# Kernel tuning notes

Measured on AMD Instinct MI355X. Metric: run time of the kernel, lower is better.

## Reference

```python
import jax, jax.numpy as jnp
import numpy as np

B, N, D, H = 64, 512, 1024, 2048


def setup_inputs() -> dict:
    key = jax.random.key(0)
    k1, k2, k3, k4, k5 = jax.random.split(key, 5)
    s1 = 1.0 / np.sqrt(D)
    s2 = 1.0 / np.sqrt(H)
    return {
        "x": jax.random.normal(k1, (B, N, D), dtype=jnp.float32),
        "W1": jax.random.uniform(k2, (H, D), jnp.float32, -s1, s1),
        "b1": jax.random.uniform(k3, (H,), jnp.float32, -s1, s1),
        "W2": jax.random.uniform(k4, (1, H), jnp.float32, -s2, s2),
        "b2": jax.random.uniform(k5, (1,), jnp.float32, -s2, s2),
    }


def reference(x, W1, b1, W2, b2):
    # energy gate: sigmoid(sum(x^2)) over feature dim -> [B, N]
    energy_weights = jax.nn.sigmoid(jnp.sum(x * x, axis=-1))
    # fused per-node MLP as one batched GEMM: relu(x @ W1^T + b1) @ W2^T + b2
    hidden = jax.nn.relu(jnp.einsum("bnd,hd->bnh", x, W1) + b1)
    score = jnp.einsum("bnh,oh->bno", hidden, W2)[..., 0] + b2[0]  # [B, N]
    attn_weights = jax.nn.sigmoid(score) * energy_weights  # [B, N]
    # diag_embed: place attn_weights on the diagonal of [B, N, N]
    filter_matrix = attn_weights[:, :, None] * jnp.eye(N, dtype=x.dtype)
    return filter_matrix, attn_weights
```

## Files before the change

### kernel.cpp

```cpp
#include <hip/hip_runtime.h>
#include <hip/hip_bf16.h>

#define Bc 64
#define Nc 512
#define Dc 1024
#define Hc 2048
#define Mc (Bc * Nc)

#define BM 256
#define BH 256
#define BK 64
#define KTILES (Dc / BK)
#define MTILES (Mc / BM)
#define HTILES (Hc / BH)
#define NSLICE (HTILES * 4)

typedef __attribute__((ext_vector_type(8))) short bf16x8;
typedef __attribute__((ext_vector_type(4))) float f32x4;

__device__ __forceinline__ unsigned short f2bf(float f) {
    unsigned u = __float_as_uint(f);
    u += 0x7FFFu + ((u >> 16) & 1u);
    return (unsigned short)(u >> 16);
}

__device__ __forceinline__ void stage16(const void* g, void* l) {
    __builtin_amdgcn_global_load_lds(
        (const __attribute__((address_space(1))) unsigned int*)g,
        (__attribute__((address_space(3))) unsigned int*)l,
        16, 0, 0);
}

__global__ void __launch_bounds__(256) cast_fused(
    const float* __restrict__ x, const float* __restrict__ w1,
    unsigned short* __restrict__ xb, unsigned short* __restrict__ w1b,
    float* __restrict__ energy)
{
    const int tid = threadIdx.x;
    if (blockIdx.x < Mc / 8) {
        const int row0 = blockIdx.x * 8 + (tid >> 6) * 2;
        const int lane = tid & 63;
        const float4* s0 = (const float4*)(x + (size_t)row0 * Dc);
        const float4* s1 = (const float4*)(x + (size_t)(row0 + 1) * Dc);
        ushort4* d0 = (ushort4*)(xb + (size_t)row0 * Dc);
        ushort4* d1 = (ushort4*)(xb + (size_t)(row0 + 1) * Dc);
        float4 v0[4], v1[4];
        #pragma unroll
        for (int j = 0; j < 4; ++j) v0[j] = s0[lane + j * 64];
        #pragma unroll
        for (int j = 0; j < 4; ++j) v1[j] = s1[lane + j * 64];
        float a = 0.0f, bsum = 0.0f;
        #pragma unroll
        for (int j = 0; j < 4; ++j) {
            ushort4 o;
            o.x = f2bf(v0[j].x); o.y = f2bf(v0[j].y);
            o.z = f2bf(v0[j].z); o.w = f2bf(v0[j].w);
            d0[lane + j * 64] = o;
            a += v0[j].x * v0[j].x + v0[j].y * v0[j].y +
                 v0[j].z * v0[j].z + v0[j].w * v0[j].w;
        }
        #pragma unroll
        for (int j = 0; j < 4; ++j) {
            ushort4 o;
            o.x = f2bf(v1[j].x); o.y = f2bf(v1[j].y);
            o.z = f2bf(v1[j].z); o.w = f2bf(v1[j].w);
            d1[lane + j * 64] = o;
            bsum += v1[j].x * v1[j].x + v1[j].y * v1[j].y +
                    v1[j].z * v1[j].z + v1[j].w * v1[j].w;
        }
        #pragma unroll
        for (int m = 1; m < 64; m <<= 1) {
            a    += __shfl_xor(a, m);
            bsum += __shfl_xor(bsum, m);
        }
        if (lane == 0) {
            energy[row0]     = 1.0f / (1.0f + expf(-a));
            energy[row0 + 1] = 1.0f / (1.0f + expf(-bsum));
        }
    } else {
        const size_t i = (size_t)(blockIdx.x - Mc / 8) * 256 + tid;
        const float4 v = ((const float4*)w1)[i];
        ushort4 o;
        o.x = f2bf(v.x); o.y = f2bf(v.y); o.z = f2bf(v.z); o.w = f2bf(v.w);
        ((ushort4*)w1b)[i] = o;
    }
}

__global__ void __launch_bounds__(512, 2) fused_gemm_score(
    const unsigned short* __restrict__ xb,
    const unsigned short* __restrict__ w1b,
    const float* __restrict__ b1,
    const float* __restrict__ w2,
    float* __restrict__ score_part,
    float* __restrict__ zf)
{
    extern __shared__ __attribute__((aligned(16))) unsigned short lds[];

    const int tid  = threadIdx.x;
    const int lane = tid & 63;
    const int wid  = tid >> 6;
    const int wr   = wid >> 2;
    const int wc   = wid & 3;
    const int l15  = lane & 15;
    const int l4   = lane >> 4;

    const int b  = blockIdx.x;
    const int wg = (b & 7) * (MTILES * HTILES / 8) + (b >> 3);
    const int mt = wg >> 3;
    const int ht = wg & 7;
    const int m0 = mt * BM;
    const int h0 = ht * BH;

    float b1v[4], w2v[4];
    #pragma unroll
    for (int n = 0; n < 4; ++n) {
        const int h = h0 + wc * 64 + n * 16 + l15;
        b1v[n] = b1[h];
        w2v[n] = w2[h];
    }

    const int srow    = tid >> 3;
    const int scol_sw = ((((tid & 7) * 16) ^ ((srow & 7) << 4)) >> 1);

    unsigned short* A0p = lds;
    #define LDSBUF(buf, mat) (A0p + (buf) * 32768 + (mat) * 16384)

    const int swz   = (l15 & 7) << 4;
    const int offk0 = ((l4 * 16) ^ swz);
    const int offk1 = ((64 + l4 * 16) ^ swz);
    const int arow  = (wr * 128 + l15) * 128;
    const int brow  = (wc * 64 + l15) * 128;

#define RD_A(dst, bf, mh) { \
    _Pragma("unroll") for (int mf = 0; mf < 4; ++mf) { \
        dst[mf][0] = *(const bf16x8*)((char*)LDSBUF(bf, 0) + arow + ((mh)*64 + mf*16) * 128 + offk0); \
        dst[mf][1] = *(const bf16x8*)((char*)LDSBUF(bf, 0) + arow + ((mh)*64 + mf*16) * 128 + offk1); } }
#define RD_B(dst, bf, nh) { \
    _Pragma("unroll") for (int nf = 0; nf < 2; ++nf) { \
        dst[nf][0] = *(const bf16x8*)((char*)LDSBUF(bf, 1) + brow + ((nh)*32 + nf*16) * 128 + offk0); \
        dst[nf][1] = *(const bf16x8*)((char*)LDSBUF(bf, 1) + brow + ((nh)*32 + nf*16) * 128 + offk1); } }

#define MMQ(av, bv, mh, nh) { \
    _Pragma("unroll") for (int mf = 0; mf < 4; ++mf) \
    _Pragma("unroll") for (int nf = 0; nf < 2; ++nf) { \
        acc[(mh)*4+mf][(nh)*2+nf] = __builtin_amdgcn_mfma_f32_16x16x32_bf16( \
            av[mf][0], bv[nf][0], acc[(mh)*4+mf][(nh)*2+nf], 0, 0, 0); \
        acc[(mh)*4+mf][(nh)*2+nf] = __builtin_amdgcn_mfma_f32_16x16x32_bf16( \
            av[mf][1], bv[nf][1], acc[(mh)*4+mf][(nh)*2+nf], 0, 0, 0); } }

    f32x4 acc[8][4];
    #pragma unroll
    for (int m = 0; m < 8; ++m)
        #pragma unroll
        for (int n = 0; n < 4; ++n) acc[m][n] = (f32x4)(0.0f);

    f32x4* zbase = zf ? (f32x4*)(zf + (size_t)b * 16384 + tid * 4) : nullptr;
    const f32x4 zero4 = (f32x4)(0.0f);

    #pragma unroll
    for (int c = 0; c < 4; ++c) {
        stage16(xb  + (size_t)(m0 + c * 64 + srow) * Dc + scol_sw,
                ((char*)LDSBUF(0, 0)) + c * 8192 + tid * 16);
        stage16(w1b + (size_t)(h0 + c * 64 + srow) * Dc + scol_sw,
                ((char*)LDSBUF(0, 1)) + c * 8192 + tid * 16);
    }
    __syncthreads();

    int cur = 0;
    for (int kt = 0; kt < KTILES; ++kt) {
        if (kt + 1 < KTILES) {
            const int k0 = (kt + 1) * BK;
            const int nb = cur ^ 1;
            #pragma unroll
            for (int c = 0; c < 4; ++c) {
                stage16(xb  + (size_t)(m0 + c * 64 + srow) * Dc + k0 + scol_sw,
                        ((char*)LDSBUF(nb, 0)) + c * 8192 + tid * 16);
                stage16(w1b + (size_t)(h0 + c * 64 + srow) * Dc + k0 + scol_sw,
                        ((char*)LDSBUF(nb, 1)) + c * 8192 + tid * 16);
            }
        }

        if (zbase && kt >= 8)
            __builtin_nontemporal_store(zero4, zbase + (size_t)(kt - 8) * 512);

        bf16x8 a0[4][2], a1[4][2], b0[2][2], b1f[2][2];

        RD_A(a0, cur, 0); RD_B(b0, cur, 0);
        RD_B(b1f, cur, 1);
        MMQ(a0, b0, 0, 0);
        RD_A(a1, cur, 1);
        MMQ(a0, b1f, 0, 1);
        MMQ(a1, b1f, 1, 1);
        MMQ(a1, b0, 1, 0);

        __syncthreads();
        cur ^= 1;
    }

    float sp[8][4];
    #pragma unroll
    for (int m = 0; m < 8; ++m)
        #pragma unroll
        for (int j = 0; j < 4; ++j) sp[m][j] = 0.0f;
    #pragma unroll
    for (int n = 0; n < 4; ++n)
        #pragma unroll
        for (int m = 0; m < 8; ++m)
            #pragma unroll
            for (int j = 0; j < 4; ++j) {
                float v = acc[m][n][j] + b1v[n];
                v = v > 0.0f ? v : 0.0f;
                sp[m][j] += v * w2v[n];
            }

    #pragma unroll
    for (int m = 0; m < 8; ++m)
        #pragma unroll
        for (int j = 0; j < 4; ++j) {
            float v = sp[m][j];
            v += __shfl_xor(v, 1);
            v += __shfl_xor(v, 2);
            v += __shfl_xor(v, 4);
            v += __shfl_xor(v, 8);
            sp[m][j] = v;
        }

    if (l15 == 0) {
        const size_t base = (size_t)(ht * 4 + wc) * Mc;
        #pragma unroll
        for (int m = 0; m < 8; ++m)
            #pragma unroll
            for (int j = 0; j < 4; ++j) {
                const int row = m0 + wr * 128 + m * 16 + l4 * 4 + j;
                score_part[base + row] = sp[m][j];
            }
    }
}

__global__ void __launch_bounds__(256) finalize_scatter(
    const float* __restrict__ score_part, const float* __restrict__ energy,
    const float* __restrict__ b2, float* __restrict__ out)
{
    const int row = blockIdx.x * 256 + threadIdx.x;
    float s = b2[0];
    #pragma unroll
    for (int g = 0; g < NSLICE; ++g) s += score_part[(size_t)g * Mc + row];
    const float attn = (1.0f / (1.0f + expf(-s))) * energy[row];
    const int bb = row >> 9;
    const int n  = row & (Nc - 1);
    out[(size_t)bb * Nc * Nc + (size_t)n * (Nc + 1)] = attn;
    out[(size_t)Bc * Nc * Nc + row] = attn;
}

__global__ void __launch_bounds__(256) finalize_full(
    const float* __restrict__ score_part, const float* __restrict__ energy,
    const float* __restrict__ b2, float* __restrict__ out)
{
    const int row = blockIdx.x * 2 + (threadIdx.x >> 7);
    const int t   = threadIdx.x & 127;

    float s = b2[0];
    #pragma unroll
    for (int g = 0; g < NSLICE; ++g) s += score_part[(size_t)g * Mc + row];
    const float attn = (1.0f / (1.0f + expf(-s))) * energy[row];

    const int n = row & (Nc - 1);
    float4 z = make_float4(0.0f, 0.0f, 0.0f, 0.0f);
    if (t == (n >> 2)) ((float*)&z)[n & 3] = attn;
    ((float4*)(out + (size_t)row * Nc))[t] = z;
    if (t == 0) out[(size_t)Bc * Nc * Nc + row] = attn;
}

extern "C" void kernel_launch(void* const* d_in, const int* in_sizes, int n_in,
                              void* d_out, int out_size, void* d_ws, size_t ws_size,
                              hipStream_t stream) {
    const float* x  = (const float*)d_in[0];
    const float* W1 = (const float*)d_in[1];
    const float* b1 = (const float*)d_in[2];
    const float* W2 = (const float*)d_in[3];
    const float* b2 = (const float*)d_in[4];
    float* out = (float*)d_out;

    const size_t xb_bytes = (size_t)Mc * Dc * 2;
    const size_t w1_bytes = (size_t)Hc * Dc * 2;
    const size_t e_bytes  = (size_t)Mc * 4;
    const size_t s_bytes  = (size_t)NSLICE * Mc * 4;

    char* ws = (char*)d_ws;
    unsigned short* xb;
    bool xb_in_out = false;
    if (ws_size >= xb_bytes + w1_bytes + e_bytes + s_bytes + 256) {
        xb = (unsigned short*)ws; ws += xb_bytes;
    } else {
        xb = (unsigned short*)d_out;
        xb_in_out = true;
    }
    unsigned short* w1b = (unsigned short*)ws; ws += w1_bytes;
    float* energy = (float*)ws; ws += e_bytes;
    float* score  = (float*)ws; ws += s_bytes;

    const int w1_blocks = (Hc * Dc / 4) / 256;
    cast_fused<<<Mc / 8 + w1_blocks, 256, 0, stream>>>(x, W1, xb, w1b, energy);
    fused_gemm_score<<<MTILES * HTILES, 512, 131072, stream>>>(
        xb, w1b, b1, W2, score, xb_in_out ? nullptr : out);
    if (xb_in_out)
        finalize_full<<<Mc / 2, 256, 0, stream>>>(score, energy, b2, out);
    else
        finalize_scatter<<<Mc / 256, 256, 0, stream>>>(score, energy, b2, out);
}
```

Baseline: 151.7 us.

## Use 4 waves with 128x128 per-wave tiles in fused GEMM-score kernel

Restructures the 256x256 block GEMM from 8 waves of 128x64 to 4 waves of 128x128 each, raising per-wave register reuse of B fragments (read once per k-step, reused across 8 A row groups). Staging is redistributed over 256 threads, the zero-store of the output is spread across all 16 k-tiles, and the number of score partial slices halves. This doubles accumulator registers per thread (256 floats) and drops to one workgroup per CU with fewer waves to hide latency, risking spills or lower occupancy.

New measurement: 169.8 us. 11.9% more time.

```diff
diff --git a/kernel.cpp b/kernel.cpp
--- a/kernel.cpp
+++ b/kernel.cpp
@@ -13,7 +13,7 @@
 #define KTILES (Dc / BK)
 #define MTILES (Mc / BM)
 #define HTILES (Hc / BH)
-#define NSLICE (HTILES * 4)
+#define NSLICE (HTILES * 2)
 
 typedef __attribute__((ext_vector_type(8))) short bf16x8;
 typedef __attribute__((ext_vector_type(4))) float f32x4;
@@ -86,7 +86,7 @@
     }
 }
 
-__global__ void __launch_bounds__(512, 2) fused_gemm_score(
+__global__ void __launch_bounds__(256, 1) fused_gemm_score(
     const unsigned short* __restrict__ xb,
     const unsigned short* __restrict__ w1b,
     const float* __restrict__ b1,
@@ -94,13 +94,13 @@
     float* __restrict__ score_part,
     float* __restrict__ zf)
 {
-    extern __shared__ __attribute__((aligned(16))) unsigned short lds[];
+    extern __shared__ __attribute__((aligned(16))) char lds[];
 
     const int tid  = threadIdx.x;
     const int lane = tid & 63;
     const int wid  = tid >> 6;
-    const int wr   = wid >> 2;
-    const int wc   = wid & 3;
+    const int wr   = wid >> 1;
+    const int wc   = wid & 1;
     const int l15  = lane & 15;
     const int l4   = lane >> 4;
 
@@ -111,10 +111,10 @@
     const int m0 = mt * BM;
     const int h0 = ht * BH;
 
-    float b1v[4], w2v[4];
-    #pragma unroll
-    for (int n = 0; n < 4; ++n) {
-        const int h = h0 + wc * 64 + n * 16 + l15;
+    float b1v[8], w2v[8];
+    #pragma unroll
+    for (int n = 0; n < 8; ++n) {
+        const int h = h0 + wc * 128 + n * 16 + l15;
         b1v[n] = b1[h];
         w2v[n] = w2[h];
     }
@@ -122,76 +122,71 @@
     const int srow    = tid >> 3;
     const int scol_sw = ((((tid & 7) * 16) ^ ((srow & 7) << 4)) >> 1);
 
-    unsigned short* A0p = lds;
-    #define LDSBUF(buf, mat) (A0p + (buf) * 32768 + (mat) * 16384)
+#define LDSA(bf) (lds + (bf) * 65536)
+#define LDSB(bf) (lds + (bf) * 65536 + 32768)
+
+#define STG_A(bf, kt) { \
+    const unsigned short* _g = xb + (size_t)(m0 + srow) * Dc + (kt) * BK + scol_sw; \
+    _Pragma("unroll") for (int c = 0; c < 8; ++c) \
+        stage16(_g + (size_t)c * 32 * Dc, LDSA(bf) + c * 4096 + tid * 16); }
+#define STG_B(bf, kt) { \
+    const unsigned short* _g = w1b + (size_t)(h0 + srow) * Dc + (kt) * BK + scol_sw; \
+    _Pragma("unroll") for (int c = 0; c < 8; ++c) \
+        stage16(_g + (size_t)c * 32 * Dc, LDSB(bf) + c * 4096 + tid * 16); }
 
     const int swz   = (l15 & 7) << 4;
     const int offk0 = ((l4 * 16) ^ swz);
     const int offk1 = ((64 + l4 * 16) ^ swz);
-    const int arow  = (wr * 128 + l15) * 128;
-    const int brow  = (wc * 64 + l15) * 128;
-
-#define RD_A(dst, bf, mh) { \
-    _Pragma("unroll") for (int mf = 0; mf < 4; ++mf) { \
-        dst[mf][0] = *(const bf16x8*)((char*)LDSBUF(bf, 0) + arow + ((mh)*64 + mf*16) * 128 + offk0); \
-        dst[mf][1] = *(const bf16x8*)((char*)LDSBUF(bf, 0) + arow + ((mh)*64 + mf*16) * 128 + offk1); } }
-#define RD_B(dst, bf, nh) { \
-    _Pragma("unroll") for (int nf = 0; nf < 2; ++nf) { \
-        dst[nf][0] = *(const bf16x8*)((char*)LDSBUF(bf, 1) + brow + ((nh)*32 + nf*16) * 128 + offk0); \
-        dst[nf][1] = *(const bf16x8*)((char*)LDSBUF(bf, 1) + brow + ((nh)*32 + nf*16) * 128 + offk1); } }
-
-#define MMQ(av, bv, mh, nh) { \
-    _Pragma("unroll") for (int mf = 0; mf < 4; ++mf) \
-    _Pragma("unroll") for (int nf = 0; nf < 2; ++nf) { \
-        acc[(mh)*4+mf][(nh)*2+nf] = __builtin_amdgcn_mfma_f32_16x16x32_bf16( \
-            av[mf][0], bv[nf][0], acc[(mh)*4+mf][(nh)*2+nf], 0, 0, 0); \
-        acc[(mh)*4+mf][(nh)*2+nf] = __builtin_amdgcn_mfma_f32_16x16x32_bf16( \
-            av[mf][1], bv[nf][1], acc[(mh)*4+mf][(nh)*2+nf], 0, 0, 0); } }
-
-    f32x4 acc[8][4];
+
+#define RD_A2(dst, bf, p) { \
+    _Pragma("unroll") for (int r = 0; r < 2; ++r) { \
+        dst[r][0] = *(const bf16x8*)(LDSA(bf) + (wr * 128 + ((p)*2+r) * 16 + l15) * 128 + offk0); \
+        dst[r][1] = *(const bf16x8*)(LDSA(bf) + (wr * 128 + ((p)*2+r) * 16 + l15) * 128 + offk1); } }
+#define RD_B8(bf) { \
+    _Pragma("unroll") for (int n = 0; n < 8; ++n) { \
+        bfr[n][0] = *(const bf16x8*)(LDSB(bf) + (wc * 128 + n * 16 + l15) * 128 + offk0); \
+        bfr[n][1] = *(const bf16x8*)(LDSB(bf) + (wc * 128 + n * 16 + l15) * 128 + offk1); } }
+
+#define MM2(av, p) { \
+    _Pragma("unroll") for (int r = 0; r < 2; ++r) \
+    _Pragma("unroll") for (int n = 0; n < 8; ++n) { \
+        acc[(p)*2+r][n] = __builtin_amdgcn_mfma_f32_16x16x32_bf16( \
+            av[r][0], bfr[n][0], acc[(p)*2+r][n], 0, 0, 0); \
+        acc[(p)*2+r][n] = __builtin_amdgcn_mfma_f32_16x16x32_bf16( \
+            av[r][1], bfr[n][1], acc[(p)*2+r][n], 0, 0, 0); } }
+
+    bf16x8 bfr[8][2], aP[2][2], aQ[2][2];
+    f32x4  acc[8][8];
     #pragma unroll
     for (int m = 0; m < 8; ++m)
         #pragma unroll
-        for (int n = 0; n < 4; ++n) acc[m][n] = (f32x4)(0.0f);
+        for (int n = 0; n < 8; ++n) acc[m][n] = (f32x4)(0.0f);
 
     f32x4* zbase = zf ? (f32x4*)(zf + (size_t)b * 16384 + tid * 4) : nullptr;
     const f32x4 zero4 = (f32x4)(0.0f);
 
-    #pragma unroll
-    for (int c = 0; c < 4; ++c) {
-        stage16(xb  + (size_t)(m0 + c * 64 + srow) * Dc + scol_sw,
-                ((char*)LDSBUF(0, 0)) + c * 8192 + tid * 16);
-        stage16(w1b + (size_t)(h0 + c * 64 + srow) * Dc + scol_sw,
-                ((char*)LDSBUF(0, 1)) + c * 8192 + tid * 16);
-    }
+    STG_A(0, 0); STG_B(0, 0);
     __syncthreads();
 
     int cur = 0;
     for (int kt = 0; kt < KTILES; ++kt) {
         if (kt + 1 < KTILES) {
-            const int k0 = (kt + 1) * BK;
             const int nb = cur ^ 1;
-            #pragma unroll
-            for (int c = 0; c < 4; ++c) {
-                stage16(xb  + (size_t)(m0 + c * 64 + srow) * Dc + k0 + scol_sw,
-                        ((char*)LDSBUF(nb, 0)) + c * 8192 + tid * 16);
-                stage16(w1b + (size_t)(h0 + c * 64 + srow) * Dc + k0 + scol_sw,
-                        ((char*)LDSBUF(nb, 1)) + c * 8192 + tid * 16);
-            }
-        }
-
-        if (zbase && kt >= 8)
-            __builtin_nontemporal_store(zero4, zbase + (size_t)(kt - 8) * 512);
-
-        bf16x8 a0[4][2], a1[4][2], b0[2][2], b1f[2][2];
-
-        RD_A(a0, cur, 0); RD_B(b0, cur, 0);
-        RD_B(b1f, cur, 1);
-        MMQ(a0, b0, 0, 0);
-        RD_A(a1, cur, 1);
-        MMQ(a0, b1f, 0, 1);
-        MMQ(a1, b1f, 1, 1);
-        MMQ(a1, b0, 1, 0);
+            STG_A(nb, kt + 1); STG_B(nb, kt + 1);
+        }
+
+        if (zbase)
+            __builtin_nontemporal_store(zero4, zbase + (size_t)kt * 256);
+
+        RD_B8(cur);
+        RD_A2(aP, cur, 0);
+        RD_A2(aQ, cur, 1);
+        MM2(aP, 0);
+        RD_A2(aP, cur, 2);
+        MM2(aQ, 1);
+        RD_A2(aQ, cur, 3);
+        MM2(aP, 2);
+        MM2(aQ, 3);
 
         __syncthreads();
         cur ^= 1;
@@ -203,7 +198,7 @@
         #pragma unroll
         for (int j = 0; j < 4; ++j) sp[m][j] = 0.0f;
     #pragma unroll
-    for (int n = 0; n < 4; ++n)
+    for (int n = 0; n < 8; ++n)
         #pragma unroll
         for (int m = 0; m < 8; ++m)
             #pragma unroll
@@ -226,7 +221,7 @@
         }
 
     if (l15 == 0) {
-        const size_t base = (size_t)(ht * 4 + wc) * Mc;
+        const size_t base = (size_t)(ht * 2 + wc) * Mc;
         #pragma unroll
         for (int m = 0; m < 8; ++m)
             #pragma unroll
@@ -301,7 +296,7 @@
 
     const int w1_blocks = (Hc * Dc / 4) / 256;
     cast_fused<<<Mc / 8 + w1_blocks, 256, 0, stream>>>(x, W1, xb, w1b, energy);
-    fused_gemm_score<<<MTILES * HTILES, 512, 131072, stream>>>(
+    fused_gemm_score<<<MTILES * HTILES, 256, 131072, stream>>>(
         xb, w1b, b1, W2, score, xb_in_out ? nullptr : out);
     if (xb_in_out)
         finalize_full<<<Mc / 2, 256, 0, stream>>>(score, energy, b2, out);
```
